# Kernel tuning notes

Measured on AMD Instinct MI355X. Metric: run time of the kernel, lower is better.

## Reference

```python
import jax, jax.numpy as jnp
import numpy as np

DECAY = 0.99
EPS = 1e-05
COMMIT_COST = 0.25


def setup_inputs() -> dict:
    key = jax.random.key(0)
    k1, k2 = jax.random.split(key)
    z = jax.random.normal(k1, (32, 256, 64, 64), dtype=jnp.float32)
    codebook = jax.random.normal(k2, (512, 256), dtype=jnp.float32)
    n_i = jnp.zeros((512,), dtype=jnp.float32)
    e_i = codebook  # register_buffer('e_i', codebook.data.clone())
    return {"z": z, "codebook": codebook, "n_i": n_i, "e_i": e_i}


def reference(z, codebook, n_i, e_i):
    K, D = codebook.shape
    b = z.shape[0]
    flat = z.reshape(-1, D)  # [N, D]

    dist = (
        jnp.sum(flat * flat, axis=1, keepdims=True)
        + jnp.sum(codebook * codebook, axis=1)
        - 2.0 * (flat @ codebook.T)
    )  # [N, K]
    encoding = jnp.argmin(dist, axis=1)  # [N]

    # one-hot matmul gather == direct gather
    code = codebook[encoding].reshape(z.shape)

    # EMA codebook update (training path, no-grad in the original)
    counts = jax.ops.segment_sum(
        jnp.ones((flat.shape[0],), dtype=flat.dtype), encoding, num_segments=K
    )  # idx.sum(0)
    code_update = jax.ops.segment_sum(flat, encoding, num_segments=K)  # idx.T @ flat
    n_new = DECAY * n_i + (1.0 - DECAY) * counts
    n_new = (n_new + EPS) / (b + K * EPS) * b  # Laplace smoothing (uses batch size b)
    e_new = DECAY * e_i + (1.0 - DECAY) * code_update
    codebook_new = e_new / n_new[:, None]

    commitment_loss = COMMIT_COST * jnp.mean(
        (z - jax.lax.stop_gradient(code)) ** 2
    )
    # straight-through estimator
    code_ste = z + jax.lax.stop_gradient(code - z)
    return (code_ste, commitment_loss, encoding, codebook_new, n_new, e_new)
```

## Files before the change

### kernel.cpp

```cpp
#include <hip/hip_runtime.h>
#include <cfloat>

#define NROWS 131072
#define DIM 256
#define KCODES 512
#define DECAYF 0.99f
#define OMDECAYF 0.01f
#define EPSF 1e-5f
#define BATCHF 32.0f

#define CHUNK 128
#define ROWMASK 0x1FFFF

#define BMW 16
#define BMB 64
#define PLANE_STRIDE (KCODES * DIM)
#define PLANE_BYTES (PLANE_STRIDE * 2)
#define PC2 16
#define NPIECE (KCODES / PC2)
#define PIECE_H_BYTES 8192
#define SBUF_HALF 16384

typedef __attribute__((ext_vector_type(8))) _Float16 half8;
typedef __attribute__((ext_vector_type(4))) float f32x4;


__device__ __forceinline__ void gload_lds16(const void* g, void* l) {
  __builtin_amdgcn_global_load_lds(
      (const __attribute__((address_space(1))) unsigned int*)g,
      (__attribute__((address_space(3))) unsigned int*)l, 16, 0, 0);
}

__global__ __launch_bounds__(256) void cnorm_kernel(const float* __restrict__ cb,
                                                    const float* __restrict__ e_i,
                                                    float* __restrict__ cnorm,
                                                    float* __restrict__ en_out,
                                                    unsigned short* __restrict__ planes,
                                                    int* __restrict__ counts,
                                                    int* __restrict__ off,
                                                    float* __restrict__ loss_acc) {
  int k = blockIdx.x;
  int t = threadIdx.x;
  if (t == 0) {
    counts[k] = 0;
    off[k] = 0;
    if (k == 0) loss_acc[0] = 0.f;
  }
  size_t idx = (size_t)k * DIM + t;
  float v = cb[idx];
  en_out[idx] = DECAYF * e_i[idx];
  _Float16 h = (_Float16)v;
  float r1 = v - (float)h;
  _Float16 m = (_Float16)r1;
  unsigned short hb, mb;
  __builtin_memcpy(&hb, &h, 2);
  __builtin_memcpy(&mb, &m, 2);
  int tile = k >> 4, cl = k & 15;
  int kc = t >> 5, lk = (t >> 3) & 3, j = t & 7;
  size_t faddr = ((size_t)((tile * 8 + kc) * 64 + lk * 16 + cl)) * 8 + j;
  planes[faddr] = hb;
  planes[PLANE_STRIDE + faddr] = mb;
  float s = v * v;
  for (int o = 32; o > 0; o >>= 1) s += __shfl_down(s, o);
  __shared__ float p[4];
  if ((t & 63) == 0) p[t >> 6] = s;
  __syncthreads();
  if (t == 0) cnorm[k] = (p[0] + p[1]) + (p[2] + p[3]);
}

__global__ __launch_bounds__(256, 4) void argmin_kernel(
    const float* __restrict__ z, const unsigned short* __restrict__ planes,
    const float* __restrict__ cnorm, const float* __restrict__ cb,
    int* __restrict__ enc_int, float* __restrict__ enc_out,
    int* __restrict__ counts, float* __restrict__ code_out,
    float* __restrict__ loss_acc) {
  __shared__ __align__(16) unsigned char sbuf[2 * SBUF_HALF];
  __shared__ float cn_s[KCODES];
  __shared__ int hist[KCODES];
  __shared__ int sm_enc[BMB];
  __shared__ float lds_loss;

  const int tid = threadIdx.x;
  const int w = tid >> 6;
  const int l = tid & 63;
  const int lc = l & 15;
  const int lk = l >> 4;

  hist[tid] = 0;
  hist[tid + 256] = 0;
  cn_s[tid] = cnorm[tid];
  cn_s[tid + 256] = cnorm[tid + 256];
  if (tid == 0) lds_loss = 0.f;

  half8 a_h[8], a_m[8];
  float zn = 0.f;
  {
    int row = blockIdx.x * BMB + w * BMW + lc;
    const float* zr = z + (size_t)row * DIM;
#pragma unroll
    for (int ch = 0; ch < 8; ++ch) {
      float4 v0 = *(const float4*)&zr[ch * 32 + lk * 8];
      float4 v1 = *(const float4*)&zr[ch * 32 + lk * 8 + 4];
      float vv[8] = {v0.x, v0.y, v0.z, v0.w, v1.x, v1.y, v1.z, v1.w};
      half8 hh, mm;
#pragma unroll
      for (int j = 0; j < 8; ++j) {
        float f = vv[j];
        zn += f * f;
        _Float16 hb = (_Float16)f;
        float r1 = f - (float)hb;
        hh[j] = hb;
        mm[j] = (_Float16)r1;
      }
      a_h[ch] = hh; a_m[ch] = mm;
    }
  }
  zn += __shfl_xor(zn, 16);
  zn += __shfl_xor(zn, 32);

  float minv[4];
  int mini[4];
#pragma unroll
  for (int q = 0; q < 4; ++q) { minv[q] = FLT_MAX; mini[q] = 0; }

  const unsigned char* gplanes = (const unsigned char*)planes;

#define STAGE(p, b)                                                              \
  {                                                                              \
    const unsigned char* gh = gplanes + (size_t)(p) * PIECE_H_BYTES;             \
    unsigned char* lb = &sbuf[(b) * SBUF_HALF];                                  \
    _Pragma("unroll")                                                            \
    for (int q = 0; q < 4; ++q) {                                                \
      int c = w * 4 + q;                                                         \
      const unsigned char* g = (w < 2)                                           \
          ? gh + c * 1024 + l * 16                                               \
          : gh + PLANE_BYTES + (c - 8) * 1024 + l * 16;                          \
      gload_lds16(g, lb + c * 1024);                                             \
    }                                                                            \
  }

  STAGE(0, 0);
  __syncthreads();

#pragma unroll 1
  for (int p = 0; p < NPIECE; ++p) {
    const int cur = p & 1;
    if (p + 1 < NPIECE) STAGE(p + 1, cur ^ 1);

    const int lbase = cur * SBUF_HALF;
    f32x4 acc_a = {0.f, 0.f, 0.f, 0.f};
    f32x4 acc_b = {0.f, 0.f, 0.f, 0.f};
#pragma unroll
    for (int kc = 0; kc < 8; ++kc) {
      int o = lbase + kc * 1024 + l * 16;
      half8 bh = *(const half8*)&sbuf[o];
      half8 bm = *(const half8*)&sbuf[o + 8192];
      acc_a = __builtin_amdgcn_mfma_f32_16x16x32_f16(a_h[kc], bh, acc_a, 0, 0, 0);
      acc_b = __builtin_amdgcn_mfma_f32_16x16x32_f16(a_m[kc], bh, acc_b, 0, 0, 0);
      acc_a = __builtin_amdgcn_mfma_f32_16x16x32_f16(a_h[kc], bm, acc_a, 0, 0, 0);
    }
    {
      int code = p * PC2 + lc;
      float cn = cn_s[code];
#pragma unroll
      for (int q = 0; q < 4; ++q) {
        float s0 = cn - 2.f * (acc_a[q] + acc_b[q]);
        if (s0 < minv[q]) { minv[q] = s0; mini[q] = code; }
      }
    }
    __syncthreads();
  }
#undef STAGE


  float lsum = 0.f;
#pragma unroll
  for (int q = 0; q < 4; ++q) {
    float v = minv[q];
    int idx = mini[q];
    for (int o = 1; o < 16; o <<= 1) {
      float ov = __shfl_xor(v, o);
      int oi = __shfl_xor(idx, o);
      if (ov < v || (ov == v && oi < idx)) { v = ov; idx = oi; }
    }
    float znq = __shfl(zn, lk * 4 + q);
    if (lc == 0) {
      int rloc = w * BMW + lk * 4 + q;
      int row = blockIdx.x * BMB + rloc;
      enc_int[row] = idx;
      enc_out[row] = (float)idx;
      sm_enc[rloc] = idx;
      atomicAdd(&hist[idx], 1);
      lsum += znq + v;
    }
  }
  {
    float val = (lc == 0) ? lsum : 0.f;
    val += __shfl_xor(val, 16);
    val += __shfl_xor(val, 32);
    if (l == 0) atomicAdd(&lds_loss, val);
  }
  __syncthreads();

  {
    const float4* cb4 = (const float4*)cb;
    float4* out4 = (float4*)code_out;
    int base = blockIdx.x * (BMB * (DIM / 4));
#pragma unroll
    for (int it = 0; it < 16; ++it) {
      int idx = it * 256 + tid;
      int k = sm_enc[idx >> 6];
      out4[base + idx] = cb4[k * (DIM / 4) + (idx & 63)];
    }
  }

  {
    int h0 = hist[tid];
    if (h0) atomicAdd(&counts[tid], h0);
    int h1 = hist[tid + 256];
    if (h1) atomicAdd(&counts[tid + 256], h1);
  }
  if (tid == 0) atomicAdd(loss_acc, lds_loss);
}

__global__ __launch_bounds__(256) void scatter_kernel(
    const int* __restrict__ enc, const int* __restrict__ counts,
    int* __restrict__ off, int* __restrict__ rowlist) {
  __shared__ int lcnt[KCODES];
  __shared__ int lbase[KCODES];
  __shared__ int pref[KCODES];
  int tid = threadIdx.x;
  int row = blockIdx.x * 256 + tid;
  lcnt[tid] = 0;
  lcnt[tid + 256] = 0;
  pref[tid] = counts[tid];
  pref[tid + 256] = counts[tid + 256];
  __syncthreads();
  int k = enc[row];
  int p = atomicAdd(&lcnt[k], 1);
  for (int o = 1; o < KCODES; o <<= 1) {
    int v0 = (tid >= o) ? pref[tid - o] : 0;
    int v1 = (tid + 256 >= o) ? pref[tid + 256 - o] : 0;
    __syncthreads();
    pref[tid] += v0;
    pref[tid + 256] += v1;
    __syncthreads();
  }
  int c0 = lcnt[tid];
  if (c0) lbase[tid] = (pref[tid] - counts[tid]) + atomicAdd(&off[tid], c0);
  int c1 = lcnt[tid + 256];
  if (c1) lbase[tid + 256] = (pref[tid + 256] - counts[tid + 256]) + atomicAdd(&off[tid + 256], c1);
  __syncthreads();
  rowlist[lbase[k] + p] = (k << 17) | row;
}

__global__ __launch_bounds__(256) void chunk_sum_kernel(
    const float* __restrict__ z, const int* __restrict__ rowlist,
    float* __restrict__ en_out) {
  __shared__ int rl[CHUNK];
  int tid = threadIdx.x;
  int d = tid;
  if (tid < CHUNK) rl[tid] = rowlist[blockIdx.x * CHUNK + tid];
  __syncthreads();
  int cur = rl[0] >> 17;
  float s = 0.f;
  for (int i = 0; i < CHUNK; i += 4) {
    int p0 = rl[i + 0], p1 = rl[i + 1], p2 = rl[i + 2], p3 = rl[i + 3];
    float v0 = z[(size_t)(p0 & ROWMASK) * DIM + d];
    float v1 = z[(size_t)(p1 & ROWMASK) * DIM + d];
    float v2 = z[(size_t)(p2 & ROWMASK) * DIM + d];
    float v3 = z[(size_t)(p3 & ROWMASK) * DIM + d];
    int k;
    k = p0 >> 17;
    if (k != cur) { atomicAdd(&en_out[(size_t)cur * DIM + d], OMDECAYF * s); s = 0.f; cur = k; }
    s += v0;
    k = p1 >> 17;
    if (k != cur) { atomicAdd(&en_out[(size_t)cur * DIM + d], OMDECAYF * s); s = 0.f; cur = k; }
    s += v1;
    k = p2 >> 17;
    if (k != cur) { atomicAdd(&en_out[(size_t)cur * DIM + d], OMDECAYF * s); s = 0.f; cur = k; }
    s += v2;
    k = p3 >> 17;
    if (k != cur) { atomicAdd(&en_out[(size_t)cur * DIM + d], OMDECAYF * s); s = 0.f; cur = k; }
    s += v3;
  }
  atomicAdd(&en_out[(size_t)cur * DIM + d], OMDECAYF * s);
}

__global__ __launch_bounds__(256) void finalize_kernel(
    const float* __restrict__ en, const int* __restrict__ counts,
    const float* __restrict__ n_i, float* __restrict__ nn_out,
    float* __restrict__ cbn_out, const float* __restrict__ loss_acc,
    float* __restrict__ loss_out) {
  int k = blockIdx.x;
  int d = threadIdx.x;
  float nn = DECAYF * n_i[k] + OMDECAYF * (float)counts[k];
  nn = (nn + EPSF) / (BATCHF + (float)KCODES * EPSF) * BATCHF;
  if (d == 0) nn_out[k] = nn;
  size_t idx = (size_t)k * DIM + d;
  cbn_out[idx] = en[idx] / nn;
  if (k == 0 && d == 0) loss_out[0] = 0.25f * loss_acc[0] / 33554432.0f;
}

extern "C" void kernel_launch(void* const* d_in, const int* in_sizes, int n_in,
                              void* d_out, int out_size, void* d_ws, size_t ws_size,
                              hipStream_t stream) {
  const float* z = (const float*)d_in[0];
  const float* cb = (const float*)d_in[1];
  const float* n_i = (const float*)d_in[2];
  const float* e_i = (const float*)d_in[3];

  float* out = (float*)d_out;
  float* out_code = out;
  float* out_loss = out + 33554432;
  float* out_enc = out + 33554433;
  float* out_cbn = out + 33685505;
  float* out_nn = out + 33816577;
  float* out_en = out + 33817089;

  char* ws = (char*)d_ws;
  float* cnorm = (float*)(ws + 0);
  int* counts = (int*)(ws + 2048);
  float* loss_acc = (float*)(ws + 4096);
  int* off = (int*)(ws + 6144);
  int* enc_int = (int*)(ws + 12288);
  int* rowlist = (int*)(ws + 536576);
  unsigned short* planes = (unsigned short*)(ws + 536576);

  cnorm_kernel<<<KCODES, 256, 0, stream>>>(cb, e_i, cnorm, out_en, planes,
                                           counts, off, loss_acc);
  argmin_kernel<<<NROWS / BMB, 256, 0, stream>>>(z, planes, cnorm, cb, enc_int,
                                                 out_enc, counts, out_code, loss_acc);
  scatter_kernel<<<NROWS / 256, 256, 0, stream>>>(enc_int, counts, off, rowlist);
  chunk_sum_kernel<<<NROWS / CHUNK, 256, 0, stream>>>(z, rowlist, out_en);
  finalize_kernel<<<KCODES, 256, 0, stream>>>(out_en, counts, n_i, out_nn,
                                              out_cbn, loss_acc, out_loss);
}
```

Measured before the change: 361.3 us.

## Process two row tiles per wave in argmin and vectorize chunk sums

Each wave now computes distances for 32 rows instead of 16, reusing each codebook fragment loaded from LDS across two row tiles, and the occupancy hint is lowered to 3 to fit the extra registers. The chunk-sum kernel switches to float4 loads, with four row groups interleaved over the chunk. This aims to cut LDS traffic and sync overhead per MFMA and raise memory efficiency in the segment sum. In exchange it raises register pressure, lowers occupancy, and adds more atomics.

```diff
diff --git a/kernel.cpp b/kernel.cpp
--- a/kernel.cpp
+++ b/kernel.cpp
@@ -12,8 +12,9 @@
 #define CHUNK 128
 #define ROWMASK 0x1FFFF
 
-#define BMW 16
-#define BMB 64
+#define RT 2
+#define BMW (RT * 16)
+#define BMB (4 * BMW)
 #define PLANE_STRIDE (KCODES * DIM)
 #define PLANE_BYTES (PLANE_STRIDE * 2)
 #define PC2 16
@@ -68,7 +69,7 @@
   if (t == 0) cnorm[k] = (p[0] + p[1]) + (p[2] + p[3]);
 }
 
-__global__ __launch_bounds__(256, 4) void argmin_kernel(
+__global__ __launch_bounds__(256, 3) void argmin_kernel(
     const float* __restrict__ z, const unsigned short* __restrict__ planes,
     const float* __restrict__ cnorm, const float* __restrict__ cb,
     int* __restrict__ enc_int, float* __restrict__ enc_out,
@@ -92,11 +93,13 @@
   cn_s[tid + 256] = cnorm[tid + 256];
   if (tid == 0) lds_loss = 0.f;
 
-  half8 a_h[8], a_m[8];
-  float zn = 0.f;
-  {
-    int row = blockIdx.x * BMB + w * BMW + lc;
+  half8 a_h[RT][8], a_m[RT][8];
+  float zn[RT];
+#pragma unroll
+  for (int rt = 0; rt < RT; ++rt) {
+    int row = blockIdx.x * BMB + w * BMW + rt * 16 + lc;
     const float* zr = z + (size_t)row * DIM;
+    float zacc = 0.f;
 #pragma unroll
     for (int ch = 0; ch < 8; ++ch) {
       float4 v0 = *(const float4*)&zr[ch * 32 + lk * 8];
@@ -106,22 +109,25 @@
 #pragma unroll
       for (int j = 0; j < 8; ++j) {
         float f = vv[j];
-        zn += f * f;
+        zacc += f * f;
         _Float16 hb = (_Float16)f;
         float r1 = f - (float)hb;
         hh[j] = hb;
         mm[j] = (_Float16)r1;
       }
-      a_h[ch] = hh; a_m[ch] = mm;
-    }
-  }
-  zn += __shfl_xor(zn, 16);
-  zn += __shfl_xor(zn, 32);
-
-  float minv[4];
-  int mini[4];
-#pragma unroll
-  for (int q = 0; q < 4; ++q) { minv[q] = FLT_MAX; mini[q] = 0; }
+      a_h[rt][ch] = hh; a_m[rt][ch] = mm;
+    }
+    zacc += __shfl_xor(zacc, 16);
+    zacc += __shfl_xor(zacc, 32);
+    zn[rt] = zacc;
+  }
+
+  float minv[RT][4];
+  int mini[RT][4];
+#pragma unroll
+  for (int rt = 0; rt < RT; ++rt)
+#pragma unroll
+    for (int q = 0; q < 4; ++q) { minv[rt][q] = FLT_MAX; mini[rt][q] = 0; }
 
   const unsigned char* gplanes = (const unsigned char*)planes;
 
@@ -148,24 +154,31 @@
     if (p + 1 < NPIECE) STAGE(p + 1, cur ^ 1);
 
     const int lbase = cur * SBUF_HALF;
-    f32x4 acc_a = {0.f, 0.f, 0.f, 0.f};
-    f32x4 acc_b = {0.f, 0.f, 0.f, 0.f};
+    f32x4 acc_a0 = {0.f, 0.f, 0.f, 0.f};
+    f32x4 acc_b0 = {0.f, 0.f, 0.f, 0.f};
+    f32x4 acc_a1 = {0.f, 0.f, 0.f, 0.f};
+    f32x4 acc_b1 = {0.f, 0.f, 0.f, 0.f};
 #pragma unroll
     for (int kc = 0; kc < 8; ++kc) {
       int o = lbase + kc * 1024 + l * 16;
       half8 bh = *(const half8*)&sbuf[o];
       half8 bm = *(const half8*)&sbuf[o + 8192];
-      acc_a = __builtin_amdgcn_mfma_f32_16x16x32_f16(a_h[kc], bh, acc_a, 0, 0, 0);
-      acc_b = __builtin_amdgcn_mfma_f32_16x16x32_f16(a_m[kc], bh, acc_b, 0, 0, 0);
-      acc_a = __builtin_amdgcn_mfma_f32_16x16x32_f16(a_h[kc], bm, acc_a, 0, 0, 0);
+      acc_a0 = __builtin_amdgcn_mfma_f32_16x16x32_f16(a_h[0][kc], bh, acc_a0, 0, 0, 0);
+      acc_a1 = __builtin_amdgcn_mfma_f32_16x16x32_f16(a_h[1][kc], bh, acc_a1, 0, 0, 0);
+      acc_b0 = __builtin_amdgcn_mfma_f32_16x16x32_f16(a_m[0][kc], bh, acc_b0, 0, 0, 0);
+      acc_b1 = __builtin_amdgcn_mfma_f32_16x16x32_f16(a_m[1][kc], bh, acc_b1, 0, 0, 0);
+      acc_a0 = __builtin_amdgcn_mfma_f32_16x16x32_f16(a_h[0][kc], bm, acc_a0, 0, 0, 0);
+      acc_a1 = __builtin_amdgcn_mfma_f32_16x16x32_f16(a_h[1][kc], bm, acc_a1, 0, 0, 0);
     }
     {
       int code = p * PC2 + lc;
       float cn = cn_s[code];
 #pragma unroll
       for (int q = 0; q < 4; ++q) {
-        float s0 = cn - 2.f * (acc_a[q] + acc_b[q]);
-        if (s0 < minv[q]) { minv[q] = s0; mini[q] = code; }
+        float s0 = cn - 2.f * (acc_a0[q] + acc_b0[q]);
+        if (s0 < minv[0][q]) { minv[0][q] = s0; mini[0][q] = code; }
+        float s1 = cn - 2.f * (acc_a1[q] + acc_b1[q]);
+        if (s1 < minv[1][q]) { minv[1][q] = s1; mini[1][q] = code; }
       }
     }
     __syncthreads();
@@ -175,23 +188,26 @@
 
   float lsum = 0.f;
 #pragma unroll
-  for (int q = 0; q < 4; ++q) {
-    float v = minv[q];
-    int idx = mini[q];
-    for (int o = 1; o < 16; o <<= 1) {
-      float ov = __shfl_xor(v, o);
-      int oi = __shfl_xor(idx, o);
-      if (ov < v || (ov == v && oi < idx)) { v = ov; idx = oi; }
-    }
-    float znq = __shfl(zn, lk * 4 + q);
-    if (lc == 0) {
-      int rloc = w * BMW + lk * 4 + q;
-      int row = blockIdx.x * BMB + rloc;
-      enc_int[row] = idx;
-      enc_out[row] = (float)idx;
-      sm_enc[rloc] = idx;
-      atomicAdd(&hist[idx], 1);
-      lsum += znq + v;
+  for (int rt = 0; rt < RT; ++rt) {
+#pragma unroll
+    for (int q = 0; q < 4; ++q) {
+      float v = minv[rt][q];
+      int idx = mini[rt][q];
+      for (int o = 1; o < 16; o <<= 1) {
+        float ov = __shfl_xor(v, o);
+        int oi = __shfl_xor(idx, o);
+        if (ov < v || (ov == v && oi < idx)) { v = ov; idx = oi; }
+      }
+      float znq = __shfl(zn[rt], lk * 4 + q);
+      if (lc == 0) {
+        int rloc = w * BMW + rt * 16 + lk * 4 + q;
+        int row = blockIdx.x * BMB + rloc;
+        enc_int[row] = idx;
+        enc_out[row] = (float)idx;
+        sm_enc[rloc] = idx;
+        atomicAdd(&hist[idx], 1);
+        lsum += znq + v;
+      }
     }
   }
   {
@@ -207,7 +223,7 @@
     float4* out4 = (float4*)code_out;
     int base = blockIdx.x * (BMB * (DIM / 4));
 #pragma unroll
-    for (int it = 0; it < 16; ++it) {
+    for (int it = 0; it < 32; ++it) {
       int idx = it * 256 + tid;
       int k = sm_enc[idx >> 6];
       out4[base + idx] = cb4[k * (DIM / 4) + (idx & 63)];
@@ -259,32 +275,34 @@
     float* __restrict__ en_out) {
   __shared__ int rl[CHUNK];
   int tid = threadIdx.x;
-  int d = tid;
+  int dq = tid & 63;
+  int g = tid >> 6;
   if (tid < CHUNK) rl[tid] = rowlist[blockIdx.x * CHUNK + tid];
   __syncthreads();
-  int cur = rl[0] >> 17;
-  float s = 0.f;
-  for (int i = 0; i < CHUNK; i += 4) {
-    int p0 = rl[i + 0], p1 = rl[i + 1], p2 = rl[i + 2], p3 = rl[i + 3];
-    float v0 = z[(size_t)(p0 & ROWMASK) * DIM + d];
-    float v1 = z[(size_t)(p1 & ROWMASK) * DIM + d];
-    float v2 = z[(size_t)(p2 & ROWMASK) * DIM + d];
-    float v3 = z[(size_t)(p3 & ROWMASK) * DIM + d];
-    int k;
-    k = p0 >> 17;
-    if (k != cur) { atomicAdd(&en_out[(size_t)cur * DIM + d], OMDECAYF * s); s = 0.f; cur = k; }
-    s += v0;
-    k = p1 >> 17;
-    if (k != cur) { atomicAdd(&en_out[(size_t)cur * DIM + d], OMDECAYF * s); s = 0.f; cur = k; }
-    s += v1;
-    k = p2 >> 17;
-    if (k != cur) { atomicAdd(&en_out[(size_t)cur * DIM + d], OMDECAYF * s); s = 0.f; cur = k; }
-    s += v2;
-    k = p3 >> 17;
-    if (k != cur) { atomicAdd(&en_out[(size_t)cur * DIM + d], OMDECAYF * s); s = 0.f; cur = k; }
-    s += v3;
-  }
-  atomicAdd(&en_out[(size_t)cur * DIM + d], OMDECAYF * s);
+  const float4* z4 = (const float4*)z;
+  int cur = rl[g] >> 17;
+  float4 s = {0.f, 0.f, 0.f, 0.f};
+#pragma unroll 4
+  for (int i = g; i < CHUNK; i += 4) {
+    int pk = rl[i];
+    int k = pk >> 17;
+    float4 v = z4[(size_t)(pk & ROWMASK) * (DIM / 4) + dq];
+    if (k != cur) {
+      float* e = &en_out[(size_t)cur * DIM + dq * 4];
+      atomicAdd(e + 0, OMDECAYF * s.x);
+      atomicAdd(e + 1, OMDECAYF * s.y);
+      atomicAdd(e + 2, OMDECAYF * s.z);
+      atomicAdd(e + 3, OMDECAYF * s.w);
+      s.x = 0.f; s.y = 0.f; s.z = 0.f; s.w = 0.f;
+      cur = k;
+    }
+    s.x += v.x; s.y += v.y; s.z += v.z; s.w += v.w;
+  }
+  float* e = &en_out[(size_t)cur * DIM + dq * 4];
+  atomicAdd(e + 0, OMDECAYF * s.x);
+  atomicAdd(e + 1, OMDECAYF * s.y);
+  atomicAdd(e + 2, OMDECAYF * s.z);
+  atomicAdd(e + 3, OMDECAYF * s.w);
 }
 
 __global__ __launch_bounds__(256) void finalize_kernel(
```

Result: slower. 462.7 us (+28.1%).
